# Optimization experiments

Measured on AMD Instinct MI355X. Metric: run time of the kernel, lower is better.

Reference implementation:

```python
import jax, jax.numpy as jnp
import numpy as np

EPS = 1e-5

def _layernorm(h, g, b):
    mu = jnp.mean(h, axis=-1, keepdims=True)
    var = jnp.mean(jnp.square(h - mu), axis=-1, keepdims=True)
    return (h - mu) * jax.lax.rsqrt(var + EPS) * g + b

def setup_inputs() -> dict:
    key = jax.random.key(0)
    ks = jax.random.split(key, 16)
    N, E, H = 100000, 500000, 128
    x = jax.random.normal(ks[0], (N, H), dtype=jnp.float32)
    edge_index = jax.random.randint(ks[1], (2, E), 0, N, dtype=jnp.int64)
    edge = jax.random.normal(ks[2], (E, H), dtype=jnp.float32)
    def lin(k, fan_in, fan_out):
        bound = 1.0 / np.sqrt(fan_in)
        k1, k2 = jax.random.split(k)
        W = jax.random.uniform(k1, (fan_in, fan_out), jnp.float32, -bound, bound)
        b = jax.random.uniform(k2, (fan_out,), jnp.float32, -bound, bound)
        return W, b
    W0, b0 = lin(ks[3], 3 * H, H)
    W1, b1 = lin(ks[4], H, H)
    W2, b2 = lin(ks[5], H, H)
    W3, b3 = lin(ks[6], H, 1)
    g0 = jnp.ones((H,), jnp.float32); be0 = jnp.zeros((H,), jnp.float32)
    g1 = jnp.ones((H,), jnp.float32); be1 = jnp.zeros((H,), jnp.float32)
    g2 = jnp.ones((H,), jnp.float32); be2 = jnp.zeros((H,), jnp.float32)
    return dict(x=x, edge_index=edge_index, edge=edge,
                W0=W0, b0=b0, g0=g0, be0=be0,
                W1=W1, b1=b1, g1=g1, be1=be1,
                W2=W2, b2=b2, g2=g2, be2=be2,
                W3=W3, b3=b3)

def reference(x, edge_index, edge, W0, b0, g0, be0, W1, b1, g1, be1, W2, b2, g2, be2, W3, b3):
    src, dst = edge_index[0], edge_index[1]
    # gather + concat: [E, 3*H]
    h = jnp.concatenate([x[src], x[dst], edge], axis=-1)
    h = jax.nn.relu(_layernorm(h @ W0 + b0, g0, be0))
    h = jax.nn.relu(_layernorm(h @ W1 + b1, g1, be1))
    h = jax.nn.relu(_layernorm(h @ W2 + b2, g2, be2))
    out = h @ W3 + b3  # [E, 1]
    return jnp.squeeze(out, axis=-1)
```

## Files before the change

### kernel.cpp

```cpp
#include <hip/hip_runtime.h>

typedef _Float16 f16;
typedef _Float16 f16x8 __attribute__((ext_vector_type(8)));
typedef _Float16 f16x4 __attribute__((ext_vector_type(4)));
typedef float    f32x4 __attribute__((ext_vector_type(4)));

static constexpr int H  = 128;
static constexpr int MT = 128;
static constexpr int PC = 40;
static constexpr int PA = 136;

__global__ __launch_bounds__(256, 2)
void edge_mlp_fused(const float* __restrict__ x,
                    const int* __restrict__ eidx,
                    const float* __restrict__ edge,
                    const float* __restrict__ W0, const float* __restrict__ b0,
                    const float* __restrict__ g0, const float* __restrict__ be0,
                    const float* __restrict__ W1, const float* __restrict__ b1,
                    const float* __restrict__ g1, const float* __restrict__ be1,
                    const float* __restrict__ W2, const float* __restrict__ b2,
                    const float* __restrict__ g2, const float* __restrict__ be2,
                    const float* __restrict__ W3, const float* __restrict__ b3,
                    float* __restrict__ out, int E)
{
    __shared__ f16   achunk[MT * PC];
    __shared__ f16   wchunk[H * PC];
    __shared__ f16   act[MT * PA];
    __shared__ int   srcoff[MT];
    __shared__ int   dstoff[MT];
    __shared__ float outbuf[MT];

    const int tid  = threadIdx.x;
    const int lane = tid & 63;
    const int wid  = tid >> 6;
    const int c    = lane & 15;
    const int g    = lane >> 4;
    const int wrow = wid * 32;
    const long long e0 = (long long)blockIdx.x * MT;

    if (tid < MT) {
        long long e = e0 + tid; if (e >= E) e = (long long)E - 1;
        srcoff[tid] = eidx[e]     * (H * 4);
        dstoff[tid] = eidx[E + e] * (H * 4);
    }

    f32x4 acc[8][2];
    #pragma unroll
    for (int t = 0; t < 8; ++t) {
        acc[t][0] = f32x4{0.f, 0.f, 0.f, 0.f};
        acc[t][1] = f32x4{0.f, 0.f, 0.f, 0.f};
    }

    auto stageW = [&](const float* __restrict__ W, int k0) {
        #pragma unroll
        for (int i = 0; i < 4; ++i) {
            int f  = i * 256 + tid;
            int n  = f & 127;
            int kq = f >> 7;
            const float* p = W + (size_t)(k0 + kq * 4) * H + n;
            f16x4 v;
            v[0] = (f16)p[0];
            v[1] = (f16)p[H];
            v[2] = (f16)p[2 * H];
            v[3] = (f16)p[3 * H];
            *(f16x4*)&wchunk[n * PC + kq * 4] = v;
        }
    };

    auto mfma_tiles = [&](const f16* __restrict__ A, int astride, int koff) {
        f16x8 a0 = *(const f16x8*)&A[(wrow + c)      * astride + koff + g * 8];
        f16x8 a1 = *(const f16x8*)&A[(wrow + 16 + c) * astride + koff + g * 8];
        #pragma unroll
        for (int t = 0; t < 8; ++t) {
            f16x8 bf = *(const f16x8*)&wchunk[(t * 16 + c) * PC + g * 8];
            acc[t][0] = __builtin_amdgcn_mfma_f32_16x16x32_f16(a0, bf, acc[t][0], 0, 0, 0);
            acc[t][1] = __builtin_amdgcn_mfma_f32_16x16x32_f16(a1, bf, acc[t][1], 0, 0, 0);
        }
    };

    auto ln_relu_store = [&](const float* __restrict__ bias,
                             const float* __restrict__ gamma,
                             const float* __restrict__ beta) {
        float mu[2][4], rs[2][4];
        #pragma unroll
        for (int t = 0; t < 8; ++t) {
            float bt = bias[t * 16 + c];
            #pragma unroll
            for (int s = 0; s < 2; ++s)
                #pragma unroll
                for (int r = 0; r < 4; ++r) acc[t][s][r] += bt;
        }
        #pragma unroll
        for (int s = 0; s < 2; ++s)
            #pragma unroll
            for (int r = 0; r < 4; ++r) {
                float v = 0.f, q = 0.f;
                #pragma unroll
                for (int t = 0; t < 8; ++t) { float a = acc[t][s][r]; v += a; q += a * a; }
                #pragma unroll
                for (int m = 1; m < 16; m <<= 1) {
                    v += __shfl_xor(v, m, 64);
                    q += __shfl_xor(q, m, 64);
                }
                float mean = v * (1.0f / H);
                float var  = q * (1.0f / H) - mean * mean;
                mu[s][r] = mean;
                rs[s][r] = rsqrtf(var + 1e-5f);
            }
        __syncthreads();
        #pragma unroll
        for (int t = 0; t < 8; ++t) {
            float gm = gamma[t * 16 + c];
            float bb = beta[t * 16 + c];
            #pragma unroll
            for (int s = 0; s < 2; ++s)
                #pragma unroll
                for (int r = 0; r < 4; ++r) {
                    float v = (acc[t][s][r] - mu[s][r]) * rs[s][r] * gm + bb;
                    v = fmaxf(v, 0.f);
                    act[(wrow + s * 16 + g * 4 + r) * PA + t * 16 + c] = (f16)v;
                }
        }
        #pragma unroll
        for (int t = 0; t < 8; ++t) {
            acc[t][0] = f32x4{0.f, 0.f, 0.f, 0.f};
            acc[t][1] = f32x4{0.f, 0.f, 0.f, 0.f};
        }
    };

    for (int kc = 0; kc < 12; ++kc) {
        __syncthreads();
        {
            int r  = tid >> 1;
            int hf = tid & 1;
            int kk = (kc & 3) * 32 + hf * 16;
            const float* p;
            if (kc < 4)      p = (const float*)((const char*)x + srcoff[r]) + kk;
            else if (kc < 8) p = (const float*)((const char*)x + dstoff[r]) + kk;
            else {
                long long e = e0 + r; if (e >= E) e = (long long)E - 1;
                p = edge + e * H + kk;
            }
            float4 v0 = ((const float4*)p)[0];
            float4 v1 = ((const float4*)p)[1];
            float4 v2 = ((const float4*)p)[2];
            float4 v3 = ((const float4*)p)[3];
            f16x8 lo, hi;
            lo[0] = (f16)v0.x; lo[1] = (f16)v0.y; lo[2] = (f16)v0.z; lo[3] = (f16)v0.w;
            lo[4] = (f16)v1.x; lo[5] = (f16)v1.y; lo[6] = (f16)v1.z; lo[7] = (f16)v1.w;
            hi[0] = (f16)v2.x; hi[1] = (f16)v2.y; hi[2] = (f16)v2.z; hi[3] = (f16)v2.w;
            hi[4] = (f16)v3.x; hi[5] = (f16)v3.y; hi[6] = (f16)v3.z; hi[7] = (f16)v3.w;
            *(f16x8*)&achunk[r * PC + hf * 16]     = lo;
            *(f16x8*)&achunk[r * PC + hf * 16 + 8] = hi;
        }
        stageW(W0, kc * 32);
        __syncthreads();
        mfma_tiles(achunk, PC, 0);
    }
    ln_relu_store(b0, g0, be0);

    for (int kc = 0; kc < 4; ++kc) {
        __syncthreads();
        stageW(W1, kc * 32);
        __syncthreads();
        mfma_tiles(act, PA, kc * 32);
    }
    ln_relu_store(b1, g1, be1);

    for (int kc = 0; kc < 4; ++kc) {
        __syncthreads();
        stageW(W2, kc * 32);
        __syncthreads();
        mfma_tiles(act, PA, kc * 32);
    }

    {
        float mu[2][4], rs[2][4];
        #pragma unroll
        for (int t = 0; t < 8; ++t) {
            float bt = b2[t * 16 + c];
            #pragma unroll
            for (int s = 0; s < 2; ++s)
                #pragma unroll
                for (int r = 0; r < 4; ++r) acc[t][s][r] += bt;
        }
        #pragma unroll
        for (int s = 0; s < 2; ++s)
            #pragma unroll
            for (int r = 0; r < 4; ++r) {
                float v = 0.f, q = 0.f;
                #pragma unroll
                for (int t = 0; t < 8; ++t) { float a = acc[t][s][r]; v += a; q += a * a; }
                #pragma unroll
                for (int m = 1; m < 16; m <<= 1) {
                    v += __shfl_xor(v, m, 64);
                    q += __shfl_xor(q, m, 64);
                }
                float mean = v * (1.0f / H);
                float var  = q * (1.0f / H) - mean * mean;
                mu[s][r] = mean;
                rs[s][r] = rsqrtf(var + 1e-5f);
            }
        float po[2][4] = {{0.f,0.f,0.f,0.f},{0.f,0.f,0.f,0.f}};
        #pragma unroll
        for (int t = 0; t < 8; ++t) {
            float gm  = g2[t * 16 + c];
            float bb  = be2[t * 16 + c];
            float w3v = W3[t * 16 + c];
            #pragma unroll
            for (int s = 0; s < 2; ++s)
                #pragma unroll
                for (int r = 0; r < 4; ++r) {
                    float v = (acc[t][s][r] - mu[s][r]) * rs[s][r] * gm + bb;
                    v = fmaxf(v, 0.f);
                    po[s][r] += v * w3v;
                }
        }
        #pragma unroll
        for (int s = 0; s < 2; ++s)
            #pragma unroll
            for (int r = 0; r < 4; ++r) {
                #pragma unroll
                for (int m = 1; m < 16; m <<= 1) po[s][r] += __shfl_xor(po[s][r], m, 64);
            }
        if (c == 0) {
            #pragma unroll
            for (int s = 0; s < 2; ++s)
                #pragma unroll
                for (int r = 0; r < 4; ++r)
                    outbuf[wrow + s * 16 + g * 4 + r] = po[s][r];
        }
    }
    __syncthreads();
    if (tid < MT) {
        long long e = e0 + tid;
        if (e < E) out[e] = outbuf[tid] + b3[0];
    }
}

extern "C" void kernel_launch(void* const* d_in, const int* in_sizes, int n_in,
                              void* d_out, int out_size, void* d_ws, size_t ws_size,
                              hipStream_t stream)
{
    const float* x    = (const float*)d_in[0];
    const int*   eidx = (const int*)d_in[1];
    const float* edge = (const float*)d_in[2];
    const float* W0   = (const float*)d_in[3];
    const float* b0   = (const float*)d_in[4];
    const float* g0   = (const float*)d_in[5];
    const float* be0  = (const float*)d_in[6];
    const float* W1   = (const float*)d_in[7];
    const float* b1   = (const float*)d_in[8];
    const float* g1   = (const float*)d_in[9];
    const float* be1  = (const float*)d_in[10];
    const float* W2   = (const float*)d_in[11];
    const float* b2   = (const float*)d_in[12];
    const float* g2   = (const float*)d_in[13];
    const float* be2  = (const float*)d_in[14];
    const float* W3   = (const float*)d_in[15];
    const float* b3   = (const float*)d_in[16];
    float*       out  = (float*)d_out;

    const int E = in_sizes[1] / 2;
    const int grid = (E + MT - 1) / MT;

    hipLaunchKernelGGL(edge_mlp_fused, dim3(grid), dim3(256), 0, stream,
                       x, eidx, edge,
                       W0, b0, g0, be0,
                       W1, b1, g1, be1,
                       W2, b2, g2, be2,
                       W3, b3, out, E);
}
```

Measured before the change: 575.6 us.

## Prefetch next A/W chunks into registers and XOR-swizzle activation tile

Global loads for the next K-chunk of gathered inputs and weights are issued into registers before the MFMA work on the current chunk, so load latency overlaps compute. The padded activation buffer becomes an unpadded XOR-swizzled layout, which frees LDS, and launch bounds rise to 3 blocks per CU for more occupancy. The per-block index table, the output buffer and one barrier in the layernorm are removed, and outputs are written directly with float4 stores. Register prefetch buffers together with the higher occupancy target risk register pressure or spills.

New measurement: 681.9 us. 18.5% more time.

```diff
diff --git a/kernel.cpp b/kernel.cpp
--- a/kernel.cpp
+++ b/kernel.cpp
@@ -8,9 +8,14 @@
 static constexpr int H  = 128;
 static constexpr int MT = 128;
 static constexpr int PC = 40;
-static constexpr int PA = 136;
-
-__global__ __launch_bounds__(256, 2)
+
+__device__ __forceinline__ void wg_barrier() {
+    asm volatile("s_waitcnt lgkmcnt(0)" ::: "memory");
+    __builtin_amdgcn_s_barrier();
+    asm volatile("" ::: "memory");
+}
+
+__global__ __launch_bounds__(256, 3)
 void edge_mlp_fused(const float* __restrict__ x,
                     const int* __restrict__ eidx,
                     const float* __restrict__ edge,
@@ -23,12 +28,9 @@
                     const float* __restrict__ W3, const float* __restrict__ b3,
                     float* __restrict__ out, int E)
 {
-    __shared__ f16   achunk[MT * PC];
-    __shared__ f16   wchunk[H * PC];
-    __shared__ f16   act[MT * PA];
-    __shared__ int   srcoff[MT];
-    __shared__ int   dstoff[MT];
-    __shared__ float outbuf[MT];
+    __shared__ __align__(16) f16 achunk[MT * PC];
+    __shared__ __align__(16) f16 wchunk[H * PC];
+    __shared__ __align__(16) f16 act[MT * H];
 
     const int tid  = threadIdx.x;
     const int lane = tid & 63;
@@ -38,11 +40,12 @@
     const int wrow = wid * 32;
     const long long e0 = (long long)blockIdx.x * MT;
 
-    if (tid < MT) {
-        long long e = e0 + tid; if (e >= E) e = (long long)E - 1;
-        srcoff[tid] = eidx[e]     * (H * 4);
-        dstoff[tid] = eidx[E + e] * (H * 4);
-    }
+    const int srow = tid >> 1;
+    const int hf   = tid & 1;
+    long long er = e0 + srow; if (er >= E) er = (long long)E - 1;
+    const float* psrc = x    + (size_t)eidx[er]     * H + hf * 16;
+    const float* pdst = x    + (size_t)eidx[E + er] * H + hf * 16;
+    const float* pedg = edge + (size_t)er           * H + hf * 16;
 
     f32x4 acc[8][2];
     #pragma unroll
@@ -51,25 +54,65 @@
         acc[t][1] = f32x4{0.f, 0.f, 0.f, 0.f};
     }
 
-    auto stageW = [&](const float* __restrict__ W, int k0) {
+    float4 apf0, apf1, apf2, apf3;
+    float  wpf[16];
+
+    auto issueA = [&](int kc) {
+        const float* b = (kc < 4) ? psrc : (kc < 8) ? pdst : pedg;
+        const float4* p = (const float4*)(b + (kc & 3) * 32);
+        apf0 = p[0]; apf1 = p[1]; apf2 = p[2]; apf3 = p[3];
+    };
+    auto writeA = [&]() {
+        f16x8 lo, hi;
+        lo[0] = (f16)apf0.x; lo[1] = (f16)apf0.y; lo[2] = (f16)apf0.z; lo[3] = (f16)apf0.w;
+        lo[4] = (f16)apf1.x; lo[5] = (f16)apf1.y; lo[6] = (f16)apf1.z; lo[7] = (f16)apf1.w;
+        hi[0] = (f16)apf2.x; hi[1] = (f16)apf2.y; hi[2] = (f16)apf2.z; hi[3] = (f16)apf2.w;
+        hi[4] = (f16)apf3.x; hi[5] = (f16)apf3.y; hi[6] = (f16)apf3.z; hi[7] = (f16)apf3.w;
+        *(f16x8*)&achunk[srow * PC + hf * 16]     = lo;
+        *(f16x8*)&achunk[srow * PC + hf * 16 + 8] = hi;
+    };
+    auto issueW = [&](const float* __restrict__ W, int k0) {
         #pragma unroll
         for (int i = 0; i < 4; ++i) {
             int f  = i * 256 + tid;
             int n  = f & 127;
             int kq = f >> 7;
             const float* p = W + (size_t)(k0 + kq * 4) * H + n;
+            wpf[i * 4 + 0] = p[0];
+            wpf[i * 4 + 1] = p[H];
+            wpf[i * 4 + 2] = p[2 * H];
+            wpf[i * 4 + 3] = p[3 * H];
+        }
+    };
+    auto writeW = [&]() {
+        #pragma unroll
+        for (int i = 0; i < 4; ++i) {
+            int f  = i * 256 + tid;
+            int n  = f & 127;
+            int kq = f >> 7;
             f16x4 v;
-            v[0] = (f16)p[0];
-            v[1] = (f16)p[H];
-            v[2] = (f16)p[2 * H];
-            v[3] = (f16)p[3 * H];
+            v[0] = (f16)wpf[i * 4 + 0];
+            v[1] = (f16)wpf[i * 4 + 1];
+            v[2] = (f16)wpf[i * 4 + 2];
+            v[3] = (f16)wpf[i * 4 + 3];
             *(f16x4*)&wchunk[n * PC + kq * 4] = v;
         }
     };
 
-    auto mfma_tiles = [&](const f16* __restrict__ A, int astride, int koff) {
-        f16x8 a0 = *(const f16x8*)&A[(wrow + c)      * astride + koff + g * 8];
-        f16x8 a1 = *(const f16x8*)&A[(wrow + 16 + c) * astride + koff + g * 8];
+    auto mfma_ach = [&]() {
+        f16x8 a0 = *(const f16x8*)&achunk[(wrow + c)      * PC + g * 8];
+        f16x8 a1 = *(const f16x8*)&achunk[(wrow + 16 + c) * PC + g * 8];
+        #pragma unroll
+        for (int t = 0; t < 8; ++t) {
+            f16x8 bf = *(const f16x8*)&wchunk[(t * 16 + c) * PC + g * 8];
+            acc[t][0] = __builtin_amdgcn_mfma_f32_16x16x32_f16(a0, bf, acc[t][0], 0, 0, 0);
+            acc[t][1] = __builtin_amdgcn_mfma_f32_16x16x32_f16(a1, bf, acc[t][1], 0, 0, 0);
+        }
+    };
+    auto mfma_act = [&](int koff) {
+        int col = (koff + g * 8) ^ ((c & 7) << 3);
+        f16x8 a0 = *(const f16x8*)&act[(wrow + c)      * H + col];
+        f16x8 a1 = *(const f16x8*)&act[(wrow + 16 + c) * H + col];
         #pragma unroll
         for (int t = 0; t < 8; ++t) {
             f16x8 bf = *(const f16x8*)&wchunk[(t * 16 + c) * PC + g * 8];
@@ -107,7 +150,6 @@
                 mu[s][r] = mean;
                 rs[s][r] = rsqrtf(var + 1e-5f);
             }
-        __syncthreads();
         #pragma unroll
         for (int t = 0; t < 8; ++t) {
             float gm = gamma[t * 16 + c];
@@ -118,7 +160,8 @@
                 for (int r = 0; r < 4; ++r) {
                     float v = (acc[t][s][r] - mu[s][r]) * rs[s][r] * gm + bb;
                     v = fmaxf(v, 0.f);
-                    act[(wrow + s * 16 + g * 4 + r) * PA + t * 16 + c] = (f16)v;
+                    int row = wrow + s * 16 + g * 4 + r;
+                    act[row * H + ((t * 16 + c) ^ ((row & 7) << 3))] = (f16)v;
                 }
         }
         #pragma unroll
@@ -128,50 +171,38 @@
         }
     };
 
+    issueA(0);
+    issueW(W0, 0);
+    #pragma unroll 1
     for (int kc = 0; kc < 12; ++kc) {
-        __syncthreads();
-        {
-            int r  = tid >> 1;
-            int hf = tid & 1;
-            int kk = (kc & 3) * 32 + hf * 16;
-            const float* p;
-            if (kc < 4)      p = (const float*)((const char*)x + srcoff[r]) + kk;
-            else if (kc < 8) p = (const float*)((const char*)x + dstoff[r]) + kk;
-            else {
-                long long e = e0 + r; if (e >= E) e = (long long)E - 1;
-                p = edge + e * H + kk;
-            }
-            float4 v0 = ((const float4*)p)[0];
-            float4 v1 = ((const float4*)p)[1];
-            float4 v2 = ((const float4*)p)[2];
-            float4 v3 = ((const float4*)p)[3];
-            f16x8 lo, hi;
-            lo[0] = (f16)v0.x; lo[1] = (f16)v0.y; lo[2] = (f16)v0.z; lo[3] = (f16)v0.w;
-            lo[4] = (f16)v1.x; lo[5] = (f16)v1.y; lo[6] = (f16)v1.z; lo[7] = (f16)v1.w;
-            hi[0] = (f16)v2.x; hi[1] = (f16)v2.y; hi[2] = (f16)v2.z; hi[3] = (f16)v2.w;
-            hi[4] = (f16)v3.x; hi[5] = (f16)v3.y; hi[6] = (f16)v3.z; hi[7] = (f16)v3.w;
-            *(f16x8*)&achunk[r * PC + hf * 16]     = lo;
-            *(f16x8*)&achunk[r * PC + hf * 16 + 8] = hi;
-        }
-        stageW(W0, kc * 32);
-        __syncthreads();
-        mfma_tiles(achunk, PC, 0);
+        wg_barrier();
+        writeA();
+        writeW();
+        if (kc < 11) { issueA(kc + 1); issueW(W0, (kc + 1) * 32); }
+        else         { issueW(W1, 0); }
+        wg_barrier();
+        mfma_ach();
     }
     ln_relu_store(b0, g0, be0);
 
+    #pragma unroll 1
     for (int kc = 0; kc < 4; ++kc) {
-        __syncthreads();
-        stageW(W1, kc * 32);
-        __syncthreads();
-        mfma_tiles(act, PA, kc * 32);
+        wg_barrier();
+        writeW();
+        if (kc < 3) issueW(W1, (kc + 1) * 32);
+        else        issueW(W2, 0);
+        wg_barrier();
+        mfma_act(kc * 32);
     }
     ln_relu_store(b1, g1, be1);
 
+    #pragma unroll 1
     for (int kc = 0; kc < 4; ++kc) {
-        __syncthreads();
-        stageW(W2, kc * 32);
-        __syncthreads();
-        mfma_tiles(act, PA, kc * 32);
+        wg_barrier();
+        writeW();
+        if (kc < 3) issueW(W2, (kc + 1) * 32);
+        wg_barrier();
+        mfma_act(kc * 32);
     }
 
     {
@@ -224,17 +255,22 @@
                 for (int m = 1; m < 16; m <<= 1) po[s][r] += __shfl_xor(po[s][r], m, 64);
             }
         if (c == 0) {
-            #pragma unroll
-            for (int s = 0; s < 2; ++s)
-                #pragma unroll
-                for (int r = 0; r < 4; ++r)
-                    outbuf[wrow + s * 16 + g * 4 + r] = po[s][r];
-        }
-    }
-    __syncthreads();
-    if (tid < MT) {
-        long long e = e0 + tid;
-        if (e < E) out[e] = outbuf[tid] + b3[0];
+            float bb3 = b3[0];
+            #pragma unroll
+            for (int s = 0; s < 2; ++s) {
+                long long eb = e0 + wrow + s * 16 + g * 4;
+                if (eb + 3 < E) {
+                    float4 o;
+                    o.x = po[s][0] + bb3; o.y = po[s][1] + bb3;
+                    o.z = po[s][2] + bb3; o.w = po[s][3] + bb3;
+                    *(float4*)(out + eb) = o;
+                } else {
+                    #pragma unroll
+                    for (int r = 0; r < 4; ++r)
+                        if (eb + r < E) out[eb + r] = po[s][r] + bb3;
+                }
+            }
+        }
     }
 }
 
```
